# Kernel optimization log

Hardware: AMD Instinct MI355X
Metric: run time of the kernel (lower is better)

## Reference

```python
import jax, jax.numpy as jnp
import numpy as np

B, S, D = 4, 2048, 512
H = 8
HD = D // H  # 64


def setup_inputs() -> dict:
    key = jax.random.key(0)
    ks = jax.random.split(key, 11)
    scale = 1.0 / np.sqrt(D)
    inp = {
        "query": jax.random.normal(ks[0], (B, S, D), dtype=jnp.float32),
        "key": jax.random.normal(ks[1], (B, S, D), dtype=jnp.float32),
        "value": jax.random.normal(ks[2], (B, S, D), dtype=jnp.float32),
        "Wq": jax.random.normal(ks[3], (D, D), dtype=jnp.float32) * scale,
        "bq": jnp.zeros((D,), dtype=jnp.float32),
        "Wk": jax.random.normal(ks[4], (D, D), dtype=jnp.float32) * scale,
        "bk": jnp.zeros((D,), dtype=jnp.float32),
        "Wv": jax.random.normal(ks[5], (D, D), dtype=jnp.float32) * scale,
        "bv": jnp.zeros((D,), dtype=jnp.float32),
        "Wo": jax.random.normal(ks[6], (D, D), dtype=jnp.float32) * scale,
        "bo": jnp.zeros((D,), dtype=jnp.float32),
    }
    return inp


def reference(query, key, value, Wq, bq, Wk, bk, Wv, bv, Wo, bo):
    # Linear projections (torch Linear: x @ W.T + b)
    q = (query @ Wq.T + bq).reshape(B, -1, H, HD).transpose(0, 2, 1, 3)  # [B,H,Sq,HD]
    k = (key   @ Wk.T + bk).reshape(B, -1, H, HD).transpose(0, 2, 1, 3)  # [B,H,Sk,HD]
    v = (value @ Wv.T + bv).reshape(B, -1, H, HD).transpose(0, 2, 1, 3)  # [B,H,Sk,HD]

    # Chunked loop in original is mathematically identical to full attention
    scores = jnp.einsum('bhqd,bhkd->bhqk', q, k) / np.sqrt(HD)  # [B,H,Sq,Sk]
    attn = jax.nn.softmax(scores, axis=-1)
    out = jnp.einsum('bhqk,bhkd->bhqd', attn, v)  # [B,H,Sq,HD]
    out = out.transpose(0, 2, 1, 3).reshape(B, -1, D)  # [B,Sq,D]
    return out @ Wo.T + bo
```

## Files before the change

kernel.cpp:

```cpp
#include <hip/hip_runtime.h>
#include <hip/hip_bf16.h>

typedef __attribute__((ext_vector_type(8))) short bf16x8;
typedef __attribute__((ext_vector_type(4))) float f32x4;
typedef __attribute__((ext_vector_type(16))) float f32x16;
typedef __attribute__((ext_vector_type(4))) unsigned int u32x4;

#define MFMA16(a, b, c) __builtin_amdgcn_mfma_f32_16x16x32_bf16((a), (b), (c), 0, 0, 0)
#define MFMA32(a, b, c) __builtin_amdgcn_mfma_f32_32x32x16_bf16((a), (b), (c), 0, 0, 0)

static constexpr int BATCH = 4, S = 2048, DMODEL = 512, H = 8, HD = 64;
static constexpr int M = BATCH * S;

#define WAIT_VM(N) asm volatile("s_waitcnt vmcnt(" #N ")" ::: "memory")
#define SCHEDB() __builtin_amdgcn_sched_barrier(0)

__device__ __forceinline__ float rexp2(float x) {
  float r;
  asm("v_exp_f32 %0, %1" : "=v"(r) : "v"(x));
  return r;
}

__device__ __forceinline__ short f2b(float f) {
  unsigned int u = __builtin_bit_cast(unsigned int, f);
  unsigned int r = (u + 0x7fffu + ((u >> 16) & 1u)) >> 16;
  return (short)r;
}

__device__ __forceinline__ bf16x8 cvt8(const float4& a, const float4& b) {
  bf16x8 r;
  r[0] = f2b(a.x); r[1] = f2b(a.y); r[2] = f2b(a.z); r[3] = f2b(a.w);
  r[4] = f2b(b.x); r[5] = f2b(b.y); r[6] = f2b(b.z); r[7] = f2b(b.w);
  return r;
}

__device__ __forceinline__ void glds16(const void* g, void* l) {
  __builtin_amdgcn_global_load_lds(
      (const __attribute__((address_space(1))) unsigned int*)g,
      (__attribute__((address_space(3))) unsigned int*)l, 16, 0, 0);
}

__global__ __launch_bounds__(256) void convert_all(
    const float* __restrict__ q, const float* __restrict__ k, const float* __restrict__ v,
    const float* __restrict__ Wq, const float* __restrict__ Wk,
    const float* __restrict__ Wv, const float* __restrict__ Wo,
    short* __restrict__ Abq, short* __restrict__ Abk, short* __restrict__ Abv,
    short* __restrict__ Wb) {
  const int bid = blockIdx.x;
  const float* src;
  short* dst;
  int i;
  if (bid < 6144) {
    const int which = bid >> 11;
    const int sub = bid & 2047;
    src = (which == 0) ? q : (which == 1) ? k : v;
    dst = (which == 0) ? Abq : (which == 1) ? Abk : Abv;
    i = (sub * 256 + threadIdx.x) * 8;
  } else {
    const int wb = bid - 6144;
    const int which = wb >> 7;
    const int sub = wb & 127;
    src = (which == 0) ? Wq : (which == 1) ? Wk : (which == 2) ? Wv : Wo;
    dst = Wb + which * (DMODEL * DMODEL);
    i = (sub * 256 + threadIdx.x) * 8;
  }
  float4 a = *(const float4*)&src[i];
  float4 b = *(const float4*)&src[i + 4];
  *(bf16x8*)&dst[i] = cvt8(a, b);
}

__global__ __launch_bounds__(256) void proj_gemm(
    const short* __restrict__ Abq, const short* __restrict__ Abk, const short* __restrict__ Abv,
    const short* __restrict__ Wb,
    const float* __restrict__ bq, const float* __restrict__ bk, const float* __restrict__ bv,
    short* __restrict__ Qp, short* __restrict__ Kp, short* __restrict__ Vp) {
  const int which = blockIdx.y;
  const short* A    = (which == 0) ? Abq : (which == 1) ? Abk : Abv;
  const short* W    = Wb + which * (DMODEL * DMODEL);
  const float* bias = (which == 0) ? bq : (which == 1) ? bk : bv;
  short* dst        = (which == 0) ? Qp : (which == 1) ? Kp : Vp;

  const int tm = blockIdx.x & 63;
  const int tn = blockIdx.x >> 6;
  const int m0 = tm * 128, n0 = tn * 128;
  const int t = threadIdx.x;
  const int lane = t & 63, w = t >> 6;
  const int g = lane >> 4, c = lane & 15;
  const int wr = w >> 1, wc = w & 1;

  __shared__ __align__(16) short SM[3][2 * 128 * 32];

  f32x4 acc[4][4];
  const f32x4 fz = {0.f, 0.f, 0.f, 0.f};
#pragma unroll
  for (int i = 0; i < 4; ++i)
#pragma unroll
    for (int j = 0; j < 4; ++j) acc[i][j] = fz;

  const short* Asrc0 = A + (m0 + w * 16 + (lane >> 2)) * DMODEL + (lane & 3) * 8;
  const short* Asrc1 = Asrc0 + 64 * DMODEL;
  const short* Bsrc0 = W + (n0 + w * 16 + (lane >> 2)) * DMODEL + (lane & 3) * 8;
  const short* Bsrc1 = Bsrc0 + 64 * DMODEL;

#pragma unroll
  for (int tt = 0; tt < 2; ++tt) {
    glds16(Asrc0 + tt * 32, &SM[tt][w * 512]);
    glds16(Asrc1 + tt * 32, &SM[tt][2048 + w * 512]);
    glds16(Bsrc0 + tt * 32, &SM[tt][4096 + w * 512]);
    glds16(Bsrc1 + tt * 32, &SM[tt][4096 + 2048 + w * 512]);
  }

  int ob0 = 0, ob1 = 1, ob2 = 2;
  for (int kt = 0; kt < 16; ++kt) {
    if (kt == 15) { WAIT_VM(0); } else { WAIT_VM(4); }
    __builtin_amdgcn_s_barrier();
    SCHEDB();
    if (kt < 14) {
      const int k0 = (kt + 2) * 32;
      glds16(Asrc0 + k0, &SM[ob2][w * 512]);
      glds16(Asrc1 + k0, &SM[ob2][2048 + w * 512]);
      glds16(Bsrc0 + k0, &SM[ob2][4096 + w * 512]);
      glds16(Bsrc1 + k0, &SM[ob2][4096 + 2048 + w * 512]);
    }
    SCHEDB();

    bf16x8 af[4], bfr[4];
#pragma unroll
    for (int i = 0; i < 4; ++i)
      af[i] = *(const bf16x8*)&SM[ob0][(wr * 64 + i * 16 + c) * 32 + g * 8];
#pragma unroll
    for (int j = 0; j < 4; ++j)
      bfr[j] = *(const bf16x8*)&SM[ob0][4096 + (wc * 64 + j * 16 + c) * 32 + g * 8];
    if (which == 2) {
#pragma unroll
      for (int i = 0; i < 4; ++i)
#pragma unroll
        for (int j = 0; j < 4; ++j)
          acc[i][j] = MFMA16(bfr[j], af[i], acc[i][j]);
    } else {
#pragma unroll
      for (int i = 0; i < 4; ++i)
#pragma unroll
        for (int j = 0; j < 4; ++j)
          acc[i][j] = MFMA16(af[i], bfr[j], acc[i][j]);
    }

    const int tmp = ob0; ob0 = ob1; ob1 = ob2; ob2 = tmp;
  }

  if (which == 2) {
#pragma unroll
    for (int j = 0; j < 4; ++j) {
#pragma unroll
      for (int r = 0; r < 4; ++r) {
        const int n = n0 + wc * 64 + j * 16 + g * 4 + r;
        const int h = n >> 6, hd = n & 63;
        const float bn = bias[n];
#pragma unroll
        for (int i = 0; i < 4; ++i) {
          const int m = m0 + wr * 64 + i * 16 + c;
          const int bb = m >> 11, s = m & (S - 1);
          dst[((bb * H + h) * HD + hd) * S + s] = f2b(acc[i][j][r] + bn);
        }
      }
    }
  } else {
#pragma unroll
    for (int i = 0; i < 4; ++i) {
#pragma unroll
      for (int j = 0; j < 4; ++j) {
        const int n = n0 + wc * 64 + j * 16 + c;
        const int h = n >> 6, hd = n & 63;
        const float bn = bias[n];
#pragma unroll
        for (int r = 0; r < 4; ++r) {
          const int m = m0 + wr * 64 + i * 16 + g * 4 + r;
          const int bb = m >> 11, s = m & (S - 1);
          dst[((bb * H + h) * S + s) * HD + hd] = f2b(acc[i][j][r] + bn);
        }
      }
    }
  }
}

__global__ __launch_bounds__(256) void out_gemm(
    const short* __restrict__ Am, const short* __restrict__ W,
    const float* __restrict__ bias, float* __restrict__ Out) {
  const int tm = blockIdx.x & 63;
  const int tn = blockIdx.x >> 6;
  const int m0 = tm * 128, n0 = tn * 128;
  const int t = threadIdx.x;
  const int lane = t & 63, w = t >> 6;
  const int g = lane >> 4, c = lane & 15;
  const int wr = w >> 1, wc = w & 1;

  __shared__ __align__(16) short SM[3][2 * 128 * 32];

  f32x4 acc[4][4];
  const f32x4 fz = {0.f, 0.f, 0.f, 0.f};
#pragma unroll
  for (int i = 0; i < 4; ++i)
#pragma unroll
    for (int j = 0; j < 4; ++j) acc[i][j] = fz;

  const short* Asrc0 = Am + (m0 + w * 16 + (lane >> 2)) * DMODEL + (lane & 3) * 8;
  const short* Asrc1 = Asrc0 + 64 * DMODEL;
  const short* Bsrc0 = W + (n0 + w * 16 + (lane >> 2)) * DMODEL + (lane & 3) * 8;
  const short* Bsrc1 = Bsrc0 + 64 * DMODEL;

#pragma unroll
  for (int tt = 0; tt < 2; ++tt) {
    glds16(Asrc0 + tt * 32, &SM[tt][w * 512]);
    glds16(Asrc1 + tt * 32, &SM[tt][2048 + w * 512]);
    glds16(Bsrc0 + tt * 32, &SM[tt][4096 + w * 512]);
    glds16(Bsrc1 + tt * 32, &SM[tt][4096 + 2048 + w * 512]);
  }

  int ob0 = 0, ob1 = 1, ob2 = 2;
  for (int kt = 0; kt < 16; ++kt) {
    if (kt == 15) { WAIT_VM(0); } else { WAIT_VM(4); }
    __builtin_amdgcn_s_barrier();
    SCHEDB();
    if (kt < 14) {
      const int k0 = (kt + 2) * 32;
      glds16(Asrc0 + k0, &SM[ob2][w * 512]);
      glds16(Asrc1 + k0, &SM[ob2][2048 + w * 512]);
      glds16(Bsrc0 + k0, &SM[ob2][4096 + w * 512]);
      glds16(Bsrc1 + k0, &SM[ob2][4096 + 2048 + w * 512]);
    }
    SCHEDB();

    bf16x8 af[4], bfr[4];
#pragma unroll
    for (int i = 0; i < 4; ++i)
      af[i] = *(const bf16x8*)&SM[ob0][(wr * 64 + i * 16 + c) * 32 + g * 8];
#pragma unroll
    for (int j = 0; j < 4; ++j)
      bfr[j] = *(const bf16x8*)&SM[ob0][4096 + (wc * 64 + j * 16 + c) * 32 + g * 8];
#pragma unroll
    for (int i = 0; i < 4; ++i)
#pragma unroll
      for (int j = 0; j < 4; ++j)
        acc[i][j] = MFMA16(af[i], bfr[j], acc[i][j]);

    const int tmp = ob0; ob0 = ob1; ob1 = ob2; ob2 = tmp;
  }

#pragma unroll
  for (int i = 0; i < 4; ++i) {
#pragma unroll
    for (int j = 0; j < 4; ++j) {
      const int n = n0 + wc * 64 + j * 16 + c;
      const float bn = bias[n];
#pragma unroll
      for (int r = 0; r < 4; ++r) {
        const int m = m0 + wr * 64 + i * 16 + g * 4 + r;
        Out[m * DMODEL + n] = acc[i][j][r] + bn;
      }
    }
  }
}

__global__ __launch_bounds__(256, 2) void attn_kernel(
    const short* __restrict__ Qp, const short* __restrict__ Kp,
    const short* __restrict__ VTp, short* __restrict__ att) {
  const int bid = blockIdx.x;
  const int swzb = (bid & 7) * 64 + (bid >> 3);
  const int qt = swzb & 15;
  const int bh = swzb >> 4;
  const int b = bh >> 3, h = bh & 7;
  const short* Q  = Qp  + bh * (S * HD);
  const char*  Kg = (const char*)(Kp  + bh * (S * HD));
  const char*  Vg = (const char*)(VTp + bh * (HD * S));

  const int t = threadIdx.x;
  const int lane = t & 63, w = t >> 6;
  const int l31 = lane & 31, hi = lane >> 5;
  const int q0 = qt * 128 + w * 32;

  __shared__ __align__(16) char smem[2 * 32768];

  const int rowi = lane >> 3;
  const char* ksrc = Kg + (w * 32 + rowi) * 128 + (((lane & 7) * 16) ^ (rowi << 4));
  const int vrow = lane >> 4;
  const char* vsrc[4];
#pragma unroll
  for (int j = 0; j < 4; ++j)
    vsrc[j] = Vg + (w * 16 + j * 4 + vrow) * 4096 +
              (((lane & 15) * 16) ^ (((j * 4 + vrow) & 7) << 4));

  bf16x8 qf[4];
#pragma unroll
  for (int ks = 0; ks < 4; ++ks)
    qf[ks] = *(const bf16x8*)&Q[(q0 + l31) * HD + ks * 16 + hi * 8];

  f32x16 o0, o1, fz16;
#pragma unroll
  for (int i = 0; i < 16; ++i) { o0[i] = 0.f; o1[i] = 0.f; fz16[i] = 0.f; }
  float lst = 0.f;

  const float SCL = 0.18033688011112042f;
  const int fswz = (l31 & 7) << 4;

  {
    char* nb = smem;
#pragma unroll
    for (int j = 0; j < 4; ++j) glds16(ksrc + j * 1024, nb + w * 4096 + j * 1024);
#pragma unroll
    for (int j = 0; j < 4; ++j) glds16(vsrc[j], nb + 16384 + w * 4096 + j * 1024);
  }

  for (int kt = 0; kt < 16; ++kt) {
    WAIT_VM(0);
    __builtin_amdgcn_s_barrier();
    SCHEDB();
    if (kt < 15) {
      char* nb = smem + ((kt + 1) & 1) * 32768;
      const size_t ko = (size_t)(kt + 1) * 16384;
      const size_t vo = (size_t)(kt + 1) * 256;
#pragma unroll
      for (int j = 0; j < 4; ++j) glds16(ksrc + ko + j * 1024, nb + w * 4096 + j * 1024);
#pragma unroll
      for (int j = 0; j < 4; ++j) glds16(vsrc[j] + vo, nb + 16384 + w * 4096 + j * 1024);
    }
    SCHEDB();

    const int cb = (kt & 1) * 32768;

    f32x16 sA, sB, sC, sD;
    __builtin_amdgcn_s_setprio(1);
    {
      const int col0 = (hi * 16) ^ fswz;
      sA = MFMA32(*(const bf16x8*)&smem[cb + l31 * 128 + col0],          qf[0], fz16);
      sB = MFMA32(*(const bf16x8*)&smem[cb + (32 + l31) * 128 + col0],   qf[0], fz16);
      sC = MFMA32(*(const bf16x8*)&smem[cb + 8192 + l31 * 128 + col0],   qf[0], fz16);
      sD = MFMA32(*(const bf16x8*)&smem[cb + 8192 + (32 + l31) * 128 + col0], qf[0], fz16);
    }
#pragma unroll
    for (int ks = 1; ks < 4; ++ks) {
      const int col = (ks * 32 + hi * 16) ^ fswz;
      sA = MFMA32(*(const bf16x8*)&smem[cb + l31 * 128 + col],          qf[ks], sA);
      sB = MFMA32(*(const bf16x8*)&smem[cb + (32 + l31) * 128 + col],   qf[ks], sB);
      sC = MFMA32(*(const bf16x8*)&smem[cb + 8192 + l31 * 128 + col],   qf[ks], sC);
      sD = MFMA32(*(const bf16x8*)&smem[cb + 8192 + (32 + l31) * 128 + col], qf[ks], sD);
    }
    __builtin_amdgcn_s_setprio(0);

#pragma unroll
    for (int i = 0; i < 16; ++i) {
      sA[i] = rexp2(sA[i] * SCL);
      sB[i] = rexp2(sB[i] * SCL);
      sC[i] = rexp2(sC[i] * SCL);
      sD[i] = rexp2(sD[i] * SCL);
    }

    float ts[16];
#pragma unroll
    for (int i = 0; i < 16; ++i) ts[i] = (sA[i] + sB[i]) + (sC[i] + sD[i]);
#pragma unroll
    for (int i = 0; i < 8; ++i) ts[i] = ts[i] + ts[i + 8];
#pragma unroll
    for (int i = 0; i < 4; ++i) ts[i] = ts[i] + ts[i + 4];
    ts[0] = (ts[0] + ts[2]) + (ts[1] + ts[3]);
    lst += ts[0] + __shfl_xor(ts[0], 32, 64);

    unsigned int wrdA[8], wrdB[8], wrdC[8], wrdD[8];
#pragma unroll
    for (int i = 0; i < 8; ++i) {
      asm("v_cvt_pk_bf16_f32 %0, %1, %2" : "=v"(wrdA[i]) : "v"(sA[2 * i]), "v"(sA[2 * i + 1]));
      asm("v_cvt_pk_bf16_f32 %0, %1, %2" : "=v"(wrdB[i]) : "v"(sB[2 * i]), "v"(sB[2 * i + 1]));
      asm("v_cvt_pk_bf16_f32 %0, %1, %2" : "=v"(wrdC[i]) : "v"(sC[2 * i]), "v"(sC[2 * i + 1]));
      asm("v_cvt_pk_bf16_f32 %0, %1, %2" : "=v"(wrdD[i]) : "v"(sD[2 * i]), "v"(sD[2 * i + 1]));
    }

    __builtin_amdgcn_s_setprio(1);
#pragma unroll
    for (int ss = 0; ss < 8; ++ss) {
      const int ks = ss & 3;
      const int i0 = (ks & 1) * 4;
      const unsigned int* lo = (ss < 4) ? ((ks < 2) ? wrdA : wrdB)
                                        : ((ks < 2) ? wrdC : wrdD);
      unsigned int a0 = lo[i0 + 0], b0 = lo[i0 + 2];
      unsigned int a1 = lo[i0 + 1], b1 = lo[i0 + 3];
      asm("v_permlane32_swap_b32 %0, %1" : "+v"(a0), "+v"(b0));
      asm("v_permlane32_swap_b32 %0, %1" : "+v"(a1), "+v"(b1));
      u32x4 fw;
      fw[0] = a0; fw[1] = a1; fw[2] = b0; fw[3] = b1;
      const bf16x8 pfrag = __builtin_bit_cast(bf16x8, fw);
      const int colv = (ss * 32 + hi * 16) ^ fswz;
      const bf16x8 va0 = *(const bf16x8*)&smem[cb + 16384 + l31 * 256 + colv];
      const bf16x8 va1 = *(const bf16x8*)&smem[cb + 16384 + (32 + l31) * 256 + colv];
      o0 = MFMA32(va0, pfrag, o0);
      o1 = MFMA32(va1, pfrag, o1);
    }
    __builtin_amdgcn_s_setprio(0);
  }

  const float inv = 1.0f / lst;
  short* arow = att + (b * S + q0 + l31) * DMODEL + h * HD;
#pragma unroll
  for (int dt = 0; dt < 2; ++dt) {
#pragma unroll
    for (int rr = 0; rr < 4; ++rr) {
      float v0 = (dt ? o1[4 * rr + 0] : o0[4 * rr + 0]) * inv;
      float v1 = (dt ? o1[4 * rr + 1] : o0[4 * rr + 1]) * inv;
      float v2 = (dt ? o1[4 * rr + 2] : o0[4 * rr + 2]) * inv;
      float v3 = (dt ? o1[4 * rr + 3] : o0[4 * rr + 3]) * inv;
      unsigned int w0, w1;
      asm("v_cvt_pk_bf16_f32 %0, %1, %2" : "=v"(w0) : "v"(v0), "v"(v1));
      asm("v_cvt_pk_bf16_f32 %0, %1, %2" : "=v"(w1) : "v"(v2), "v"(v3));
      uint2 pk2;
      pk2.x = w0; pk2.y = w1;
      *(uint2*)&arow[dt * 32 + rr * 8 + hi * 4] = pk2;
    }
  }
}

extern "C" void kernel_launch(void* const* d_in, const int* in_sizes, int n_in,
                              void* d_out, int out_size, void* d_ws, size_t ws_size,
                              hipStream_t stream) {
  const float* query = (const float*)d_in[0];
  const float* key_  = (const float*)d_in[1];
  const float* value = (const float*)d_in[2];
  const float* Wq = (const float*)d_in[3];
  const float* bq = (const float*)d_in[4];
  const float* Wk = (const float*)d_in[5];
  const float* bk = (const float*)d_in[6];
  const float* Wv = (const float*)d_in[7];
  const float* bv = (const float*)d_in[8];
  const float* Wo = (const float*)d_in[9];
  const float* bo = (const float*)d_in[10];
  float* out = (float*)d_out;

  char* ws = (char*)d_ws;
  const size_t WB_BYTES  = (size_t)4 * DMODEL * DMODEL * 2;
  const size_t MAT_BYTES = (size_t)M * DMODEL * 2;
  short* Wb  = (short*)ws;
  short* Qp  = (short*)(ws + WB_BYTES);
  short* Kp  = (short*)(ws + WB_BYTES + MAT_BYTES);
  short* Vp  = (short*)(ws + WB_BYTES + 2 * MAT_BYTES);
  short* att = (short*)(ws + WB_BYTES + 3 * MAT_BYTES);
  short* Abq = (short*)(ws + WB_BYTES + 4 * MAT_BYTES);
  short* Abk = (short*)(ws + WB_BYTES + 5 * MAT_BYTES);
  short* Abv = att;

  convert_all<<<dim3(6656), 256, 0, stream>>>(query, key_, value, Wq, Wk, Wv, Wo,
                                              Abq, Abk, Abv, Wb);
  proj_gemm<<<dim3(256, 3), 256, 0, stream>>>(Abq, Abk, Abv, Wb, bq, bk, bv, Qp, Kp, Vp);
  attn_kernel<<<dim3(512), 256, 0, stream>>>(Qp, Kp, Vp, att);
  out_gemm<<<dim3(256), 256, 0, stream>>>(att, Wb + 3 * DMODEL * DMODEL, bo, out);
}
```

Measured before the change: 93.95 us.

## Deepen out-projection GEMM pipeline to 4 stages and reswizzle attention K/V LDS

The output-projection GEMM moves from a 3-buffer to a 4-buffer LDS ring with three tiles prefetched, to hide more global-load latency, and indexes buffers with kt&3 instead of rotating variables. The attention kernel changes the K and V LDS layouts: K now stores two 64-element rows per 256-byte line with a 16-way XOR swizzle, and V uses a 16-way swizzle instead of 8-way, to reduce LDS bank conflicts on MFMA operand reads. The GEMM uses more shared memory per block, which could lower occupancy.

```diff
diff --git a/kernel.cpp b/kernel.cpp
--- a/kernel.cpp
+++ b/kernel.cpp
@@ -194,7 +194,7 @@
   const int g = lane >> 4, c = lane & 15;
   const int wr = w >> 1, wc = w & 1;
 
-  __shared__ __align__(16) short SM[3][2 * 128 * 32];
+  __shared__ __align__(16) short SM[4][2 * 128 * 32];
 
   f32x4 acc[4][4];
   const f32x4 fz = {0.f, 0.f, 0.f, 0.f};
@@ -209,41 +209,39 @@
   const short* Bsrc1 = Bsrc0 + 64 * DMODEL;
 
 #pragma unroll
-  for (int tt = 0; tt < 2; ++tt) {
+  for (int tt = 0; tt < 3; ++tt) {
     glds16(Asrc0 + tt * 32, &SM[tt][w * 512]);
     glds16(Asrc1 + tt * 32, &SM[tt][2048 + w * 512]);
     glds16(Bsrc0 + tt * 32, &SM[tt][4096 + w * 512]);
     glds16(Bsrc1 + tt * 32, &SM[tt][4096 + 2048 + w * 512]);
   }
 
-  int ob0 = 0, ob1 = 1, ob2 = 2;
+#pragma unroll 4
   for (int kt = 0; kt < 16; ++kt) {
-    if (kt == 15) { WAIT_VM(0); } else { WAIT_VM(4); }
+    if (kt == 15) { WAIT_VM(0); } else if (kt == 14) { WAIT_VM(4); } else { WAIT_VM(8); }
     __builtin_amdgcn_s_barrier();
     SCHEDB();
-    if (kt < 14) {
-      const int k0 = (kt + 2) * 32;
-      glds16(Asrc0 + k0, &SM[ob2][w * 512]);
-      glds16(Asrc1 + k0, &SM[ob2][2048 + w * 512]);
-      glds16(Bsrc0 + k0, &SM[ob2][4096 + w * 512]);
-      glds16(Bsrc1 + k0, &SM[ob2][4096 + 2048 + w * 512]);
+    if (kt < 13) {
+      const int k0 = (kt + 3) * 32;
+      glds16(Asrc0 + k0, &SM[(kt + 3) & 3][w * 512]);
+      glds16(Asrc1 + k0, &SM[(kt + 3) & 3][2048 + w * 512]);
+      glds16(Bsrc0 + k0, &SM[(kt + 3) & 3][4096 + w * 512]);
+      glds16(Bsrc1 + k0, &SM[(kt + 3) & 3][4096 + 2048 + w * 512]);
     }
     SCHEDB();
 
     bf16x8 af[4], bfr[4];
 #pragma unroll
     for (int i = 0; i < 4; ++i)
-      af[i] = *(const bf16x8*)&SM[ob0][(wr * 64 + i * 16 + c) * 32 + g * 8];
+      af[i] = *(const bf16x8*)&SM[kt & 3][(wr * 64 + i * 16 + c) * 32 + g * 8];
 #pragma unroll
     for (int j = 0; j < 4; ++j)
-      bfr[j] = *(const bf16x8*)&SM[ob0][4096 + (wc * 64 + j * 16 + c) * 32 + g * 8];
+      bfr[j] = *(const bf16x8*)&SM[kt & 3][4096 + (wc * 64 + j * 16 + c) * 32 + g * 8];
 #pragma unroll
     for (int i = 0; i < 4; ++i)
 #pragma unroll
       for (int j = 0; j < 4; ++j)
         acc[i][j] = MFMA16(af[i], bfr[j], acc[i][j]);
-
-    const int tmp = ob0; ob0 = ob1; ob1 = ob2; ob2 = tmp;
   }
 
 #pragma unroll
@@ -280,14 +278,21 @@
 
   __shared__ __align__(16) char smem[2 * 32768];
 
-  const int rowi = lane >> 3;
-  const char* ksrc = Kg + (w * 32 + rowi) * 128 + (((lane & 7) * 16) ^ (rowi << 4));
+  const char* ksrc[4];
+#pragma unroll
+  for (int j = 0; j < 4; ++j) {
+    const int rj = w * 16 + j * 4 + (lane >> 4);
+    const int tk = (lane & 15) ^ (rj & 15);
+    const int kj = 2 * rj + (tk >> 3);
+    ksrc[j] = Kg + kj * 128 + (tk & 7) * 16;
+  }
   const int vrow = lane >> 4;
   const char* vsrc[4];
 #pragma unroll
-  for (int j = 0; j < 4; ++j)
-    vsrc[j] = Vg + (w * 16 + j * 4 + vrow) * 4096 +
-              (((lane & 15) * 16) ^ (((j * 4 + vrow) & 7) << 4));
+  for (int j = 0; j < 4; ++j) {
+    const int row = w * 16 + j * 4 + vrow;
+    vsrc[j] = Vg + row * 4096 + (((lane & 15) ^ (row & 15)) * 16);
+  }
 
   bf16x8 qf[4];
 #pragma unroll
@@ -300,12 +305,16 @@
   float lst = 0.f;
 
   const float SCL = 0.18033688011112042f;
-  const int fswz = (l31 & 7) << 4;
+
+  const int kbase = (l31 >> 1) * 256;
+  const int k8 = (l31 & 1) << 3;
+  const int kx = (l31 >> 1) & 15;
+  const int vx = l31 & 15;
 
   {
     char* nb = smem;
 #pragma unroll
-    for (int j = 0; j < 4; ++j) glds16(ksrc + j * 1024, nb + w * 4096 + j * 1024);
+    for (int j = 0; j < 4; ++j) glds16(ksrc[j], nb + w * 4096 + j * 1024);
 #pragma unroll
     for (int j = 0; j < 4; ++j) glds16(vsrc[j], nb + 16384 + w * 4096 + j * 1024);
   }
@@ -319,7 +328,7 @@
       const size_t ko = (size_t)(kt + 1) * 16384;
       const size_t vo = (size_t)(kt + 1) * 256;
 #pragma unroll
-      for (int j = 0; j < 4; ++j) glds16(ksrc + ko + j * 1024, nb + w * 4096 + j * 1024);
+      for (int j = 0; j < 4; ++j) glds16(ksrc[j] + ko, nb + w * 4096 + j * 1024);
 #pragma unroll
       for (int j = 0; j < 4; ++j) glds16(vsrc[j] + vo, nb + 16384 + w * 4096 + j * 1024);
     }
@@ -330,19 +339,19 @@
     f32x16 sA, sB, sC, sD;
     __builtin_amdgcn_s_setprio(1);
     {
-      const int col0 = (hi * 16) ^ fswz;
-      sA = MFMA32(*(const bf16x8*)&smem[cb + l31 * 128 + col0],          qf[0], fz16);
-      sB = MFMA32(*(const bf16x8*)&smem[cb + (32 + l31) * 128 + col0],   qf[0], fz16);
-      sC = MFMA32(*(const bf16x8*)&smem[cb + 8192 + l31 * 128 + col0],   qf[0], fz16);
-      sD = MFMA32(*(const bf16x8*)&smem[cb + 8192 + (32 + l31) * 128 + col0], qf[0], fz16);
+      const int p0 = ((k8 | hi) ^ kx) * 16;
+      sA = MFMA32(*(const bf16x8*)&smem[cb + kbase + p0],          qf[0], fz16);
+      sB = MFMA32(*(const bf16x8*)&smem[cb + 4096 + kbase + p0],   qf[0], fz16);
+      sC = MFMA32(*(const bf16x8*)&smem[cb + 8192 + kbase + p0],   qf[0], fz16);
+      sD = MFMA32(*(const bf16x8*)&smem[cb + 12288 + kbase + p0],  qf[0], fz16);
     }
 #pragma unroll
     for (int ks = 1; ks < 4; ++ks) {
-      const int col = (ks * 32 + hi * 16) ^ fswz;
-      sA = MFMA32(*(const bf16x8*)&smem[cb + l31 * 128 + col],          qf[ks], sA);
-      sB = MFMA32(*(const bf16x8*)&smem[cb + (32 + l31) * 128 + col],   qf[ks], sB);
-      sC = MFMA32(*(const bf16x8*)&smem[cb + 8192 + l31 * 128 + col],   qf[ks], sC);
-      sD = MFMA32(*(const bf16x8*)&smem[cb + 8192 + (32 + l31) * 128 + col], qf[ks], sD);
+      const int p = ((k8 | (ks * 2 + hi)) ^ kx) * 16;
+      sA = MFMA32(*(const bf16x8*)&smem[cb + kbase + p],          qf[ks], sA);
+      sB = MFMA32(*(const bf16x8*)&smem[cb + 4096 + kbase + p],   qf[ks], sB);
+      sC = MFMA32(*(const bf16x8*)&smem[cb + 8192 + kbase + p],   qf[ks], sC);
+      sD = MFMA32(*(const bf16x8*)&smem[cb + 12288 + kbase + p],  qf[ks], sD);
     }
     __builtin_amdgcn_s_setprio(0);
 
@@ -387,9 +396,9 @@
       u32x4 fw;
       fw[0] = a0; fw[1] = a1; fw[2] = b0; fw[3] = b1;
       const bf16x8 pfrag = __builtin_bit_cast(bf16x8, fw);
-      const int colv = (ss * 32 + hi * 16) ^ fswz;
-      const bf16x8 va0 = *(const bf16x8*)&smem[cb + 16384 + l31 * 256 + colv];
-      const bf16x8 va1 = *(const bf16x8*)&smem[cb + 16384 + (32 + l31) * 256 + colv];
+      const int pv = ((ss * 2 + hi) ^ vx) * 16;
+      const bf16x8 va0 = *(const bf16x8*)&smem[cb + 16384 + l31 * 256 + pv];
+      const bf16x8 va1 = *(const bf16x8*)&smem[cb + 16384 + (32 + l31) * 256 + pv];
       o0 = MFMA32(va0, pfrag, o0);
       o1 = MFMA32(va1, pfrag, o1);
     }
```

New measurement: 94.53 us. No clear change (+0.6%).
